# Optimization experiments

Measured on AMD Instinct MI355X. Metric: run time of the kernel, lower is better.

The kernel has to match this reference:

```python
import jax, jax.numpy as jnp
import numpy as np

B, S, T = 64, 24, 96
V, E, H, A = 32000, 256, 512, 512


def setup_inputs() -> dict:
    key = jax.random.key(0)
    ks = jax.random.split(key, 16)
    captions = jax.random.randint(ks[0], (B, S, T), 0, V)
    lengths = jax.random.randint(ks[1], (B, S), 1, T + 1)
    lengths = lengths.at[0].set(T)  # ensure per-sentence max length == T (matches dynamic seq_len_k)
    update_masks = jnp.arange(T)[None, None, :] < lengths[:, :, None]  # [B,S,T] bool prefix mask
    p = lambda k, shp: jax.random.normal(k, shp, dtype=jnp.float32) * 0.05
    return dict(
        captions=captions, update_masks=update_masks,
        embed_W=p(ks[2], (V, E)),
        w_Wih=p(ks[3], (4 * H, E)), w_Whh=p(ks[4], (4 * H, H)),
        w_bih=p(ks[5], (4 * H,)), w_bhh=p(ks[6], (4 * H,)),
        s_Wih=p(ks[7], (4 * H, H)), s_Whh=p(ks[8], (4 * H, H)),
        s_bih=p(ks[9], (4 * H,)), s_bhh=p(ks[10], (4 * H,)),
        wa_Wk=p(ks[11], (A, H)), wa_Wv=p(ks[12], (1, A)),
        sa_Wk=p(ks[13], (A, H)), sa_Wv=p(ks[14], (1, A)),
    )


def _lstm_cell(x, h, c, Wih, Whh, bih, bhh):
    # torch.nn.LSTMCell gate order: i, f, g, o
    g = x @ Wih.T + bih + h @ Whh.T + bhh
    i, f, gg, o = jnp.split(g, 4, axis=-1)
    c2 = jax.nn.sigmoid(f) * c + jax.nn.sigmoid(i) * jnp.tanh(gg)
    h2 = jax.nn.sigmoid(o) * jnp.tanh(c2)
    return h2, c2


def _attn(k, Wk, Wv):
    # SelfAttention: softmax(affine(tanh(affine_k(k)))) pooled context
    z = (jnp.tanh(k @ Wk.T) @ Wv.T)[..., 0]          # [B,L]
    alpha = jax.nn.softmax(z, axis=1)
    ctx = jnp.einsum('blh,bl->bh', k, alpha)
    return ctx, alpha


def reference(captions, update_masks, embed_W, w_Wih, w_Whh, w_bih, w_bhh,
              s_Wih, s_Whh, s_bih, s_bhh, wa_Wk, wa_Wv, sa_Wk, sa_Wv):
    emb = embed_W[captions]                            # [B,S,T,E]
    bsz = captions.shape[0]
    zeros = jnp.zeros((bsz, H), jnp.float32)

    def sent_step(carry, ins):
        sh, sc, wh, wc = carry
        emb_k, m_k = ins                               # [B,T,E], [B,T]

        def word_step(c2, inp):
            wh_, wc_ = c2
            x, m = inp                                 # [B,E], [B] bool
            nh, nc = _lstm_cell(x, wh_, wc_, w_Wih, w_Whh, w_bih, w_bhh)
            m1 = m[:, None]
            # masked state update; inactive positions store 0 in word_hs
            return (jnp.where(m1, nh, wh_), jnp.where(m1, nc, wc_)), jnp.where(m1, nh, 0.0)

        (wh, wc), hs = jax.lax.scan(word_step, (wh, wc),
                                    (emb_k.transpose(1, 0, 2), m_k.T))
        word_hs = hs.transpose(1, 0, 2)                # [B,T,H]
        ctx, _ = _attn(word_hs, wa_Wk, wa_Wv)
        sh, sc = _lstm_cell(ctx, sh, sc, s_Wih, s_Whh, s_bih, s_bhh)
        return (sh, sc, wh, wc), sh

    _, sent_hs = jax.lax.scan(sent_step, (zeros, zeros, zeros, zeros),
                              (emb.transpose(1, 0, 2, 3), update_masks.transpose(1, 0, 2)))
    sent_hs = sent_hs.transpose(1, 0, 2)               # [B,S,H]
    context, alpha = _attn(sent_hs, sa_Wk, sa_Wv)
    return context, alpha
```

## Files before the change

### kernel.cpp

```cpp
#include <hip/hip_runtime.h>
#include <hip/hip_cooperative_groups.h>
#include <math.h>

namespace cg = cooperative_groups;

constexpr int kB = 64, kS = 24, kT = 96, kE = 256, kH = 512, kA = 512;
constexpr int NWG = 256, NTH = 512;
constexpr int NG = 8, GWG = 32, GB = 8;
constexpr int WHP = 516;
constexpr int HSP = 580;
constexpr int EMP = 264;
constexpr int EMB0 = 4640;
constexpr int ATP = 516;

constexpr int OFF_PUB = 0;
constexpr int OFF_SH  = OFF_PUB + 2 * NG * GWG * 128;
constexpr int OFF_HS  = OFF_SH + 2 * kB * kH;
constexpr int OFF_Z   = OFF_HS + kB * kT * kH;
constexpr int OFF_CTX = OFF_Z + kB * kT;
constexpr int OFF_SHS = OFF_CTX + kB * kH;
constexpr int OFF_Z2  = OFF_SHS + kB * kS * kH;
constexpr int OFF_FLG = (OFF_Z2 + kB * kS + 31) & ~31;

typedef float f4v __attribute__((ext_vector_type(4)));

__device__ __forceinline__ float sigmoidf(float x) { return 1.0f / (1.0f + expf(-x)); }
__device__ __forceinline__ float dot4(float4 a, float4 b) {
  return a.x * b.x + a.y * b.y + a.z * b.z + a.w * b.w;
}
__device__ __forceinline__ float2 aload2(const float* p) {
  unsigned long long u = __hip_atomic_load((const unsigned long long*)p,
                                           __ATOMIC_RELAXED, __HIP_MEMORY_SCOPE_AGENT);
  union { unsigned long long u; float2 f; } cv; cv.u = u;
  return cv.f;
}
__device__ __forceinline__ float aload1(const float* p) {
  return __hip_atomic_load(p, __ATOMIC_RELAXED, __HIP_MEMORY_SCOPE_AGENT);
}
__device__ __forceinline__ void astore(float* p, float v) {
  __hip_atomic_store(p, v, __ATOMIC_RELAXED, __HIP_MEMORY_SCOPE_AGENT);
}
__device__ __forceinline__ unsigned aloadu(const unsigned* p) {
  return __hip_atomic_load(p, __ATOMIC_RELAXED, __HIP_MEMORY_SCOPE_AGENT);
}
__device__ __forceinline__ void astoreu(unsigned* p, unsigned v) {
  __hip_atomic_store(p, v, __ATOMIC_RELAXED, __HIP_MEMORY_SCOPE_AGENT);
}
__device__ __forceinline__ unsigned l2_loadu(const unsigned* p) {
  unsigned r;
  asm volatile("global_load_dword %0, %1, off sc0\n\ts_waitcnt vmcnt(0)"
               : "=v"(r) : "v"(p) : "memory");
  return r;
}
__device__ __forceinline__ float l2_load1(const float* p) {
  float r;
  asm volatile("global_load_dword %0, %1, off sc0\n\ts_waitcnt vmcnt(0)"
               : "=v"(r) : "v"(p) : "memory");
  return r;
}
__device__ __forceinline__ float2 l2_load2(const float* p) {
  float2 r;
  asm volatile("global_load_dwordx2 %0, %1, off sc0\n\ts_waitcnt vmcnt(0)"
               : "=v"(r) : "v"(p) : "memory");
  return r;
}
__device__ __forceinline__ void l2_load8(const float* p, f4v& a, f4v& b) {
  asm volatile("global_load_dwordx4 %0, %2, off sc0\n\t"
               "global_load_dwordx4 %1, %2, off offset:16 sc0\n\t"
               "s_waitcnt vmcnt(0)"
               : "=&v"(a), "=&v"(b) : "v"(p) : "memory");
}
__device__ __forceinline__ void l2_atomic_inc(unsigned* p) {
  unsigned one = 1u;
  asm volatile("global_atomic_add %0, %1, off" :: "v"(p), "v"(one) : "memory");
}

__global__ __launch_bounds__(NTH) void ha_kernel(
    const int* __restrict__ captions, const int* __restrict__ masks,
    const float* __restrict__ embed_W,
    const float* __restrict__ w_Wih, const float* __restrict__ w_Whh,
    const float* __restrict__ w_bih, const float* __restrict__ w_bhh,
    const float* __restrict__ s_Wih, const float* __restrict__ s_Whh,
    const float* __restrict__ s_bih, const float* __restrict__ s_bhh,
    const float* __restrict__ wa_Wk, const float* __restrict__ wa_Wv,
    const float* __restrict__ sa_Wk, const float* __restrict__ sa_Wv,
    float* __restrict__ out, float* __restrict__ ws) {
  cg::grid_group grid = cg::this_grid();
  const int g = blockIdx.x, tid = threadIdx.x;
  const int jj = tid >> 6, c = tid & 63;

  float* pub = ws + OFF_PUB;
  float* sh_buf = ws + OFF_SH;
  float* hs_buf = ws + OFF_HS;
  float* z_buf = ws + OFF_Z;
  float* ctx_ws = ws + OFF_CTX;
  float* sent_hs = ws + OFF_SHS;
  float* z2_buf = ws + OFF_Z2;
  unsigned* flags = (unsigned*)(ws + OFF_FLG);
  unsigned* cntp = flags + 8192;
  unsigned* tflagA = flags + 8448;
  unsigned* tdataA = flags + 8704;
  unsigned* verdA = flags + 8960;

  __shared__ __align__(16) float whh_s[64 * WHP];
  __shared__ __align__(16) float uni[6752];
  __shared__ float bias_s[64];
  __shared__ float c_s[16][8], hown_s[16][8], sc_s[16][8];
  __shared__ unsigned mbits[24];
  __shared__ float soft_s[96], red_s[96];
  __shared__ int ibuf[4];

  {
    int idx = g * NTH + tid;
    if (idx < 2 * kB * kH) sh_buf[idx] = 0.f;
  }
  if (g == 0)
    for (int idx = tid; idx < 9216; idx += NTH) flags[idx] = 0u;
  grid.sync();

  if (tid == 0) {
    unsigned xcc;
    asm volatile("s_getreg_b32 %0, hwreg(20, 0, 32)" : "=s"(xcc));
    xcc &= 7u;
    unsigned slot = atomicAdd(&cntp[xcc * 32], 1u);
    ibuf[0] = (int)xcc; ibuf[1] = (int)slot;
  }
  grid.sync();
  __syncthreads();
  const int myxcc = ibuf[0], myslot = ibuf[1];
  unsigned cnts[8]; int px[9]; px[0] = 0;
  for (int x = 0; x < 8; ++x) { cnts[x] = aloadu(&cntp[x * 32]); px[x + 1] = px[x] + (int)cnts[x]; }
  const int rank = px[myxcc] + myslot;
  const int grp = rank >> 5, r = rank & 31;
  const int B0 = GB * grp;
  bool pure = false;
  for (int x = 0; x < 8; ++x)
    if (px[x] <= grp * 32 && grp * 32 + 32 <= px[x + 1]) pure = true;
  const bool cand = pure && (cnts[myxcc] <= 40u);
  unsigned* myflag = &flags[(grp * GWG + r) * 32];

  auto g_row = [&](int cc) { return (cc >> 4) * kH + 16 * r + (cc & 15); };

  unsigned n = 0;
  {
    unsigned* tf = &tflagA[grp * 32];
    unsigned* td = &tdataA[grp * 32];
    int ok = 0;
    if (cand && r == 0 && tid == 0) {
      *td = 0xC0FFEEu;
      asm volatile("s_waitcnt vmcnt(0)" ::: "memory");
      l2_atomic_inc(tf);
    }
    if (cand && tid == 0) {
      for (int it = 0; it < 4096; ++it) {
        if (l2_loadu(tf) >= 1u) { ok = (l2_loadu(td) == 0xC0FFEEu); break; }
        __builtin_amdgcn_s_sleep(2);
      }
    }
    if (tid == 0) {
      astoreu(&verdA[grp * 32 + r], ok ? 1u : 0u);
      asm volatile("s_waitcnt vmcnt(0)" ::: "memory");
      atomicAdd(myflag, 1u);
    }
    n = 1;
    if (tid < GWG) {
      while (aloadu(&flags[(grp * GWG + tid) * 32]) < 1u) __builtin_amdgcn_s_sleep(2);
    }
    __syncthreads();
    if (tid < GWG) red_s[tid] = (float)aloadu(&verdA[grp * 32 + tid]);
    __syncthreads();
    if (tid == 0) {
      int all = 1;
      for (int i = 0; i < GWG; ++i) all &= (red_s[i] != 0.f);
      ibuf[2] = all;
    }
    __syncthreads();
  }
  const bool l2m = (ibuf[2] != 0);

  auto mstore1 = [&](float* p, float v) { if (l2m) *p = v; else astore(p, v); };
  auto mload1 = [&](const float* p) { return l2m ? l2_load1(p) : aload1(p); };
  auto mload2 = [&](const float* p) { return l2m ? l2_load2(p) : aload2(p); };
  auto mload8 = [&](const float* p, f4v& a, f4v& b) {
    if (l2m) l2_load8(p, a, b);
    else {
      float2 t0 = aload2(p), t1 = aload2(p + 2), t2 = aload2(p + 4), t3 = aload2(p + 6);
      a = f4v{t0.x, t0.y, t1.x, t1.y}; b = f4v{t2.x, t2.y, t3.x, t3.y};
    }
  };
  auto arrive = [&]() {
    __syncthreads();
    if (tid == 0) { if (l2m) l2_atomic_inc(myflag); else atomicAdd(myflag, 1u); }
  };
  auto wait = [&](unsigned nn) {
    if (tid < GWG) {
      const unsigned* fp = &flags[(grp * GWG + tid) * 32];
      if (l2m) { while (l2_loadu(fp) < nn) __builtin_amdgcn_s_sleep(1); }
      else     { while (aloadu(fp) < nn)   __builtin_amdgcn_s_sleep(1); }
    }
    __syncthreads();
  };

  for (int idx = tid; idx < 64 * kH; idx += NTH) {
    const int c2 = idx >> 9, kk = idx & 511;
    whh_s[c2 * WHP + 4 * (((kk >> 2) + 4 * (c2 & 1)) & 127) + (kk & 3)] =
        w_Whh[(size_t)g_row(c2) * kH + kk];
  }
  if (tid < 64) bias_s[tid] = w_bih[g_row(tid)] + w_bhh[g_row(tid)];
  if (tid < 128) {
    c_s[tid >> 3][tid & 7] = 0.f; hown_s[tid >> 3][tid & 7] = 0.f; sc_s[tid >> 3][tid & 7] = 0.f;
  }
  for (int idx = tid; idx < 6752; idx += NTH) uni[idx] = 0.f;
  __syncthreads();

  auto stage_hst_pub = [&](const float* slab) {
    const int lin = tid * 8, rsm = lin >> 7, rem = lin & 127;
    const int b2 = rem >> 4, kk = (rsm << 4) | (rem & 15);
    f4v a, b4; mload8(slab + lin, a, b4);
    const int ho = kk + 4 * (kk >> 5);
    *(f4v*)&uni[b2 * HSP + ho] = a;
    *(f4v*)&uni[b2 * HSP + ho + 4] = b4;
  };
  auto stage_hst_lin = [&](const float* src) {
    const int lin = tid * 8, b2 = lin >> 9, kk = lin & 511;
    f4v a, b4; mload8(src + lin, a, b4);
    const int ho = kk + 4 * (kk >> 5);
    *(f4v*)&uni[b2 * HSP + ho] = a;
    *(f4v*)&uni[b2 * HSP + ho + 4] = b4;
  };
  auto stage_emb = [&](int s2, int t2) {
    const int b2 = tid >> 6, ch = tid & 63;
    const int cap = captions[((B0 + b2) * kS + s2) * kT + t2];
    const float4 v = *(const float4*)&embed_W[(size_t)cap * kE + 4 * ch];
    *(float4*)&uni[EMB0 + b2 * EMP + 4 * ch] = v;
  };
  float xp[8];
  auto calc_xp = [&]() {
    const float* wr = w_Wih + (size_t)g_row(c) * kE + 32 * jj;
    const float* eb = &uni[EMB0];
#pragma unroll
    for (int b2 = 0; b2 < 8; ++b2) xp[b2] = 0.f;
#pragma unroll
    for (int v = 0; v < 8; ++v) {
      const float4 w = *(const float4*)&wr[4 * v];
#pragma unroll
      for (int b2 = 0; b2 < 8; ++b2)
        xp[b2] += dot4(w, *(const float4*)&eb[b2 * EMP + 32 * jj + 4 * v]);
    }
  };

  stage_emb(0, 0);
  __syncthreads();
  calc_xp();

  int gstep = 0;
  for (int s = 0; s < kS; ++s) {
    if (tid < 24) {
      const int b2 = tid / 3, w2 = tid % 3;
      unsigned bits = 0u;
      const int base = ((B0 + b2) * kS + s) * kT + 32 * w2;
      for (int j = 0; j < 32; ++j) bits |= (masks[base + j] ? 1u : 0u) << j;
      mbits[b2 * 3 + w2] = bits;
    }
    if (s > 0) stage_hst_pub(pub + ((size_t)((gstep & 1) * NG + grp)) * 4096);
    __syncthreads();

    for (int t = 0; t < kT; ++t, ++gstep) {
      float* pubw = pub + ((size_t)(((gstep + 1) & 1) * NG + grp)) * 4096;

      float acc[8];
#pragma unroll
      for (int b2 = 0; b2 < 8; ++b2) acc[b2] = xp[b2];
      {
        const int swc = 4 * (c & 1);
        const float* wrow = &whh_s[c * WHP];
#pragma unroll 4
        for (int u = 0; u < 16; ++u) {
          const int q = 16 * jj + u;
          const float4 w = *(const float4*)&wrow[4 * ((q + swc) & 127)];
          const int hoff = 4 * q + 4 * (q >> 3);
#pragma unroll
          for (int b2 = 0; b2 < 8; ++b2)
            acc[b2] += dot4(w, *(const float4*)&uni[b2 * HSP + hoff]);
        }
      }
      __syncthreads();
#pragma unroll
      for (int b2 = 0; b2 < 8; ++b2) uni[jj * HSP + c * 9 + b2] = acc[b2];
      __syncthreads();
      float hsv = 0.f;
      if (tid < 128) {
        const int hcl = tid >> 3, b2 = tid & 7;
        float gg4[4];
#pragma unroll
        for (int g2 = 0; g2 < 4; ++g2) {
          const int c2 = g2 * 16 + hcl;
          float sum = bias_s[c2];
#pragma unroll
          for (int j = 0; j < 8; ++j) sum += uni[j * HSP + c2 * 9 + b2];
          gg4[g2] = sum;
        }
        const float cold = c_s[hcl][b2];
        const float c2v = sigmoidf(gg4[1]) * cold + sigmoidf(gg4[0]) * tanhf(gg4[2]);
        const float h2 = sigmoidf(gg4[3]) * tanhf(c2v);
        const int m = (mbits[b2 * 3 + (t >> 5)] >> (t & 31)) & 1;
        const float cn = m ? c2v : cold;
        const float hn = m ? h2 : hown_s[hcl][b2];
        c_s[hcl][b2] = cn; hown_s[hcl][b2] = hn;
        mstore1(&pubw[r * 128 + b2 * 16 + hcl], hn);
        hsv = m ? h2 : 0.f;
      }
      ++n;
      arrive();
      if (tid < 128) {
        const int hcl = tid >> 3, b2 = tid & 7;
        mstore1(&hs_buf[((size_t)(B0 + b2) * kT + t) * kH + 16 * r + hcl], hsv);
      }
      int ns = s, nt = t + 1; bool have = true;
      if (nt == kT) { nt = 0; ns = s + 1; if (ns == kS) have = false; }
      if (have) stage_emb(ns, nt);
      __syncthreads();
      if (have) calc_xp();
      wait(n);
      stage_hst_pub(pubw);
      __syncthreads();
    }

    ++n; arrive(); wait(n);

    {
      const int ab = r >> 2, t0 = (r & 3) * 24;
      const int bg = B0 + ab;
      for (int half = 0; half < 2; ++half) {
        const int tb = t0 + half * 12;
        for (int idx = tid; idx < 12 * 256; idx += NTH) {
          const int pp = idx >> 8, hh2 = (idx & 255) * 2;
          float2 v = mload2(&hs_buf[((size_t)bg * kT + tb + pp) * kH + hh2]);
          *(float2*)&uni[pp * ATP + hh2] = v;
        }
        __syncthreads();
        float dacc[12];
#pragma unroll
        for (int p = 0; p < 12; ++p) dacc[p] = 0.f;
        const float4* __restrict__ wk = (const float4*)(wa_Wk + (size_t)tid * kH);
        for (int k = 0; k < kH / 4; ++k) {
          const float4 w = wk[k];
#pragma unroll
          for (int p = 0; p < 12; ++p)
            dacc[p] += dot4(w, *(const float4*)&uni[p * ATP + 4 * k]);
        }
        const float wv = wa_Wv[tid];
        const int ln = tid & 63, wid = tid >> 6;
#pragma unroll
        for (int p = 0; p < 12; ++p) {
          float v = wv * tanhf(dacc[p]);
          v += __shfl_down(v, 32); v += __shfl_down(v, 16); v += __shfl_down(v, 8);
          v += __shfl_down(v, 4);  v += __shfl_down(v, 2);  v += __shfl_down(v, 1);
          if (ln == 0) red_s[wid * 12 + p] = v;
        }
        __syncthreads();
        if (tid < 12) {
          float sum = 0.f;
#pragma unroll
          for (int w = 0; w < 8; ++w) sum += red_s[w * 12 + tid];
          mstore1(&z_buf[bg * kT + tb + tid], sum);
        }
        __syncthreads();
      }
    }
    ++n; arrive(); wait(n);

    if (r < GB) {
      const int b2 = B0 + r;
      if (tid < kT) soft_s[tid] = mload1(&z_buf[b2 * kT + tid]);
      __syncthreads();
      float mx = -1e30f;
      for (int i = 0; i < kT; ++i) mx = fmaxf(mx, soft_s[i]);
      float den = 0.f;
      for (int i = 0; i < kT; ++i) den += expf(soft_s[i] - mx);
      __syncthreads();
      if (tid < kT) soft_s[tid] = expf(soft_s[tid] - mx) / den;
      __syncthreads();
      {
        const int h0 = tid;
        float a0 = 0.f, a1 = 0.f, a2 = 0.f, a3 = 0.f;
        for (int tt = 0; tt < kT; tt += 4) {
          a0 += soft_s[tt + 0] * mload1(&hs_buf[((size_t)b2 * kT + tt + 0) * kH + h0]);
          a1 += soft_s[tt + 1] * mload1(&hs_buf[((size_t)b2 * kT + tt + 1) * kH + h0]);
          a2 += soft_s[tt + 2] * mload1(&hs_buf[((size_t)b2 * kT + tt + 2) * kH + h0]);
          a3 += soft_s[tt + 3] * mload1(&hs_buf[((size_t)b2 * kT + tt + 3) * kH + h0]);
        }
        mstore1(&ctx_ws[b2 * kH + h0], (a0 + a1) + (a2 + a3));
      }
    }
    ++n; arrive(); wait(n);

    {
      float acc[8];
#pragma unroll
      for (int b2 = 0; b2 < 8; ++b2) acc[b2] = 0.f;
      stage_hst_lin(ctx_ws + B0 * kH);
      __syncthreads();
      {
        const float* wA = s_Wih + (size_t)g_row(c) * kH + 64 * jj;
#pragma unroll 8
        for (int u = 0; u < 16; ++u) {
          const float4 w = *(const float4*)&wA[4 * u];
          const int q = 16 * jj + u;
          const int hoff = 4 * q + 4 * (q >> 3);
#pragma unroll
          for (int b2 = 0; b2 < 8; ++b2)
            acc[b2] += dot4(w, *(const float4*)&uni[b2 * HSP + hoff]);
        }
      }
      __syncthreads();
      stage_hst_lin(sh_buf + (s & 1) * kB * kH + B0 * kH);
      __syncthreads();
      {
        const float* wB = s_Whh + (size_t)g_row(c) * kH + 64 * jj;
#pragma unroll 8
        for (int u = 0; u < 16; ++u) {
          const float4 w = *(const float4*)&wB[4 * u];
          const int q = 16 * jj + u;
          const int hoff = 4 * q + 4 * (q >> 3);
#pragma unroll
          for (int b2 = 0; b2 < 8; ++b2)
            acc[b2] += dot4(w, *(const float4*)&uni[b2 * HSP + hoff]);
        }
      }
      __syncthreads();
#pragma unroll
      for (int b2 = 0; b2 < 8; ++b2) uni[jj * HSP + c * 9 + b2] = acc[b2];
      __syncthreads();
      if (tid < 128) {
        const int hcl = tid >> 3, b2 = tid & 7;
        float gg4[4];
#pragma unroll
        for (int g2 = 0; g2 < 4; ++g2) {
          const int c2 = g2 * 16 + hcl;
          const int row = g_row(c2);
          float sum = s_bih[row] + s_bhh[row];
#pragma unroll
          for (int j = 0; j < 8; ++j) sum += uni[j * HSP + c2 * 9 + b2];
          gg4[g2] = sum;
        }
        const float c2v = sigmoidf(gg4[1]) * sc_s[hcl][b2] + sigmoidf(gg4[0]) * tanhf(gg4[2]);
        const float h2 = sigmoidf(gg4[3]) * tanhf(c2v);
        sc_s[hcl][b2] = c2v;
        const int col = 16 * r + hcl;
        mstore1(&sh_buf[((s + 1) & 1) * kB * kH + (B0 + b2) * kH + col], h2);
        mstore1(&sent_hs[((size_t)(B0 + b2) * kS + s) * kH + col], h2);
      }
    }
    ++n; arrive(); wait(n);
  }

  {
    const int pair0 = r * 6;
    for (int idx = tid; idx < 6 * 256; idx += NTH) {
      const int pp = idx >> 8, hh2 = (idx & 255) * 2;
      const int pr = pair0 + pp;
      float2 v = mload2(&sent_hs[((size_t)(B0 + pr / kS) * kS + pr % kS) * kH + hh2]);
      *(float2*)&uni[pp * ATP + hh2] = v;
    }
    __syncthreads();
    float dacc[6];
#pragma unroll
    for (int p = 0; p < 6; ++p) dacc[p] = 0.f;
    const float4* __restrict__ wk = (const float4*)(sa_Wk + (size_t)tid * kH);
    for (int k = 0; k < kH / 4; ++k) {
      const float4 w = wk[k];
#pragma unroll
      for (int p = 0; p < 6; ++p)
        dacc[p] += dot4(w, *(const float4*)&uni[p * ATP + 4 * k]);
    }
    const float wv = sa_Wv[tid];
    const int ln = tid & 63, wid = tid >> 6;
#pragma unroll
    for (int p = 0; p < 6; ++p) {
      float v = wv * tanhf(dacc[p]);
      v += __shfl_down(v, 32); v += __shfl_down(v, 16); v += __shfl_down(v, 8);
      v += __shfl_down(v, 4);  v += __shfl_down(v, 2);  v += __shfl_down(v, 1);
      if (ln == 0) red_s[wid * 6 + p] = v;
    }
    __syncthreads();
    if (tid < 6) {
      float sum = 0.f;
#pragma unroll
      for (int w = 0; w < 8; ++w) sum += red_s[w * 6 + tid];
      mstore1(&z2_buf[B0 * kS + pair0 + tid], sum);
    }
  }
  ++n; arrive(); wait(n);

  if (r < GB) {
    const int b2 = B0 + r;
    if (tid < kS) soft_s[tid] = mload1(&z2_buf[b2 * kS + tid]);
    __syncthreads();
    float mx = -1e30f;
    for (int i = 0; i < kS; ++i) mx = fmaxf(mx, soft_s[i]);
    float den = 0.f;
    for (int i = 0; i < kS; ++i) den += expf(soft_s[i] - mx);
    __syncthreads();
    if (tid < kS) {
      const float al = expf(soft_s[tid] - mx) / den;
      soft_s[tid] = al;
      out[kB * kH + b2 * kS + tid] = al;
    }
    __syncthreads();
    {
      const int h0 = tid;
      float acc2 = 0.f;
      for (int s2 = 0; s2 < kS; ++s2)
        acc2 += soft_s[s2] * mload1(&sent_hs[((size_t)b2 * kS + s2) * kH + h0]);
      out[b2 * kH + h0] = acc2;
    }
  }
}

extern "C" void kernel_launch(void* const* d_in, const int* in_sizes, int n_in,
                              void* d_out, int out_size, void* d_ws, size_t ws_size,
                              hipStream_t stream) {
  (void)in_sizes; (void)n_in; (void)out_size; (void)ws_size;
  const int* captions = (const int*)d_in[0];
  const int* masks = (const int*)d_in[1];
  const float* embed_W = (const float*)d_in[2];
  const float* w_Wih = (const float*)d_in[3];
  const float* w_Whh = (const float*)d_in[4];
  const float* w_bih = (const float*)d_in[5];
  const float* w_bhh = (const float*)d_in[6];
  const float* s_Wih = (const float*)d_in[7];
  const float* s_Whh = (const float*)d_in[8];
  const float* s_bih = (const float*)d_in[9];
  const float* s_bhh = (const float*)d_in[10];
  const float* wa_Wk = (const float*)d_in[11];
  const float* wa_Wv = (const float*)d_in[12];
  const float* sa_Wk = (const float*)d_in[13];
  const float* sa_Wv = (const float*)d_in[14];
  float* out = (float*)d_out;
  float* ws = (float*)d_ws;

  void* args[] = {&captions, &masks, &embed_W, &w_Wih, &w_Whh, &w_bih, &w_bhh,
                  &s_Wih, &s_Whh, &s_bih, &s_bhh, &wa_Wk, &wa_Wv, &sa_Wk, &sa_Wv,
                  &out, &ws};
  hipLaunchCooperativeKernel((void*)ha_kernel, dim3(NWG), dim3(NTH), args, 0, stream);
}
```

Measured before the change: 25.08 ms.

## Register-tile two gate rows per thread in word LSTM recurrence and batch L2 loads

Each thread in the per-timestep Whh matvec now computes two gate rows (c2 and c2+32) over half the K range, so every LDS load of the hidden state feeds two dot products. The two K halves are combined with a cross-half shuffle before the existing reduction. The input-projection weight slice is held in registers across timesteps instead of being reloaded from global memory each step. In the attention context loop, four L2 loads are issued back-to-back before one wait instead of four separate waits. The cost is higher register pressure from the doubled accumulators and the cached weights.

```diff
diff --git a/kernel.cpp b/kernel.cpp
--- a/kernel.cpp
+++ b/kernel.cpp
@@ -69,6 +69,17 @@
                "global_load_dwordx4 %1, %2, off offset:16 sc0\n\t"
                "s_waitcnt vmcnt(0)"
                : "=&v"(a), "=&v"(b) : "v"(p) : "memory");
+}
+__device__ __forceinline__ void l2_load4s(const float* p0, const float* p1,
+                                          const float* p2, const float* p3,
+                                          float& r0, float& r1, float& r2, float& r3) {
+  asm volatile("global_load_dword %0, %4, off sc0\n\t"
+               "global_load_dword %1, %5, off sc0\n\t"
+               "global_load_dword %2, %6, off sc0\n\t"
+               "global_load_dword %3, %7, off sc0\n\t"
+               "s_waitcnt vmcnt(0)"
+               : "=&v"(r0), "=&v"(r1), "=&v"(r2), "=&v"(r3)
+               : "v"(p0), "v"(p1), "v"(p2), "v"(p3) : "memory");
 }
 __device__ __forceinline__ void l2_atomic_inc(unsigned* p) {
   unsigned one = 1u;
@@ -87,7 +98,11 @@
     float* __restrict__ out, float* __restrict__ ws) {
   cg::grid_group grid = cg::this_grid();
   const int g = blockIdx.x, tid = threadIdx.x;
-  const int jj = tid >> 6, c = tid & 63;
+  const int jj = tid >> 6;
+  const int c = tid & 63;
+  const int half = (tid >> 5) & 1;
+  const int c2 = tid & 31;
+  const int ks = jj * 2 + half;
 
   float* pub = ws + OFF_PUB;
   float* sh_buf = ws + OFF_SH;
@@ -188,6 +203,11 @@
       a = f4v{t0.x, t0.y, t1.x, t1.y}; b = f4v{t2.x, t2.y, t3.x, t3.y};
     }
   };
+  auto mload4s = [&](const float* p0, const float* p1, const float* p2, const float* p3,
+                     float& r0, float& r1, float& r2, float& r3) {
+    if (l2m) l2_load4s(p0, p1, p2, p3, r0, r1, r2, r3);
+    else { r0 = aload1(p0); r1 = aload1(p1); r2 = aload1(p2); r3 = aload1(p3); }
+  };
   auto arrive = [&]() {
     __syncthreads();
     if (tid == 0) { if (l2m) l2_atomic_inc(myflag); else atomicAdd(myflag, 1u); }
@@ -202,15 +222,25 @@
   };
 
   for (int idx = tid; idx < 64 * kH; idx += NTH) {
-    const int c2 = idx >> 9, kk = idx & 511;
-    whh_s[c2 * WHP + 4 * (((kk >> 2) + 4 * (c2 & 1)) & 127) + (kk & 3)] =
-        w_Whh[(size_t)g_row(c2) * kH + kk];
+    const int cr = idx >> 9, kk = idx & 511;
+    whh_s[cr * WHP + 4 * (((kk >> 2) + 4 * (cr & 1)) & 127) + (kk & 3)] =
+        w_Whh[(size_t)g_row(cr) * kH + kk];
   }
   if (tid < 64) bias_s[tid] = w_bih[g_row(tid)] + w_bhh[g_row(tid)];
   if (tid < 128) {
     c_s[tid >> 3][tid & 7] = 0.f; hown_s[tid >> 3][tid & 7] = 0.f; sc_s[tid >> 3][tid & 7] = 0.f;
   }
   for (int idx = tid; idx < 6752; idx += NTH) uni[idx] = 0.f;
+  float4 wir0[4], wir1[4];
+  {
+    const float* wrA = w_Wih + (size_t)g_row(c2) * kE + 16 * ks;
+    const float* wrB = w_Wih + (size_t)g_row(c2 + 32) * kE + 16 * ks;
+#pragma unroll
+    for (int v = 0; v < 4; ++v) {
+      wir0[v] = *(const float4*)&wrA[4 * v];
+      wir1[v] = *(const float4*)&wrB[4 * v];
+    }
+  }
   __syncthreads();
 
   auto stage_hst_pub = [&](const float* slab) {
@@ -234,18 +264,19 @@
     const float4 v = *(const float4*)&embed_W[(size_t)cap * kE + 4 * ch];
     *(float4*)&uni[EMB0 + b2 * EMP + 4 * ch] = v;
   };
-  float xp[8];
+  float xp0[8], xp1[8];
   auto calc_xp = [&]() {
-    const float* wr = w_Wih + (size_t)g_row(c) * kE + 32 * jj;
-    const float* eb = &uni[EMB0];
-#pragma unroll
-    for (int b2 = 0; b2 < 8; ++b2) xp[b2] = 0.f;
-#pragma unroll
-    for (int v = 0; v < 8; ++v) {
-      const float4 w = *(const float4*)&wr[4 * v];
-#pragma unroll
-      for (int b2 = 0; b2 < 8; ++b2)
-        xp[b2] += dot4(w, *(const float4*)&eb[b2 * EMP + 32 * jj + 4 * v]);
+    const float* eb = &uni[EMB0 + 16 * ks];
+#pragma unroll
+    for (int b2 = 0; b2 < 8; ++b2) { xp0[b2] = 0.f; xp1[b2] = 0.f; }
+#pragma unroll
+    for (int v = 0; v < 4; ++v) {
+#pragma unroll
+      for (int b2 = 0; b2 < 8; ++b2) {
+        const float4 ev = *(const float4*)&eb[b2 * EMP + 4 * v];
+        xp0[b2] += dot4(wir0[v], ev);
+        xp1[b2] += dot4(wir1[v], ev);
+      }
     }
   };
 
@@ -268,25 +299,34 @@
     for (int t = 0; t < kT; ++t, ++gstep) {
       float* pubw = pub + ((size_t)(((gstep + 1) & 1) * NG + grp)) * 4096;
 
-      float acc[8];
-#pragma unroll
-      for (int b2 = 0; b2 < 8; ++b2) acc[b2] = xp[b2];
+      float acc0[8], acc1[8];
+#pragma unroll
+      for (int b2 = 0; b2 < 8; ++b2) { acc0[b2] = xp0[b2]; acc1[b2] = xp1[b2]; }
       {
-        const int swc = 4 * (c & 1);
-        const float* wrow = &whh_s[c * WHP];
-#pragma unroll 4
-        for (int u = 0; u < 16; ++u) {
-          const int q = 16 * jj + u;
-          const float4 w = *(const float4*)&wrow[4 * ((q + swc) & 127)];
+        const int swc = 4 * (c2 & 1);
+        const float* w0 = &whh_s[c2 * WHP];
+        const float* w1 = &whh_s[(c2 + 32) * WHP];
+#pragma unroll
+        for (int u = 0; u < 8; ++u) {
+          const int q = 8 * ks + u;
+          const float4 wv0 = *(const float4*)&w0[4 * ((q + swc) & 127)];
+          const float4 wv1 = *(const float4*)&w1[4 * ((q + swc) & 127)];
           const int hoff = 4 * q + 4 * (q >> 3);
 #pragma unroll
-          for (int b2 = 0; b2 < 8; ++b2)
-            acc[b2] += dot4(w, *(const float4*)&uni[b2 * HSP + hoff]);
-        }
-      }
-      __syncthreads();
-#pragma unroll
-      for (int b2 = 0; b2 < 8; ++b2) uni[jj * HSP + c * 9 + b2] = acc[b2];
+          for (int b2 = 0; b2 < 8; ++b2) {
+            const float4 hv = *(const float4*)&uni[b2 * HSP + hoff];
+            acc0[b2] += dot4(wv0, hv);
+            acc1[b2] += dot4(wv1, hv);
+          }
+        }
+      }
+      __syncthreads();
+#pragma unroll
+      for (int b2 = 0; b2 < 8; ++b2) {
+        const float t0 = acc0[b2] + __shfl_xor(acc0[b2], 32);
+        const float t1 = acc1[b2] + __shfl_xor(acc1[b2], 32);
+        uni[jj * HSP + (c2 + 32 * half) * 9 + b2] = half ? t1 : t0;
+      }
       __syncthreads();
       float hsv = 0.f;
       if (tid < 128) {
@@ -294,10 +334,10 @@
         float gg4[4];
 #pragma unroll
         for (int g2 = 0; g2 < 4; ++g2) {
-          const int c2 = g2 * 16 + hcl;
-          float sum = bias_s[c2];
-#pragma unroll
-          for (int j = 0; j < 8; ++j) sum += uni[j * HSP + c2 * 9 + b2];
+          const int cc = g2 * 16 + hcl;
+          float sum = bias_s[cc];
+#pragma unroll
+          for (int j = 0; j < 8; ++j) sum += uni[j * HSP + cc * 9 + b2];
           gg4[g2] = sum;
         }
         const float cold = c_s[hcl][b2];
@@ -331,8 +371,8 @@
     {
       const int ab = r >> 2, t0 = (r & 3) * 24;
       const int bg = B0 + ab;
-      for (int half = 0; half < 2; ++half) {
-        const int tb = t0 + half * 12;
+      for (int halfp = 0; halfp < 2; ++halfp) {
+        const int tb = t0 + halfp * 12;
         for (int idx = tid; idx < 12 * 256; idx += NTH) {
           const int pp = idx >> 8, hh2 = (idx & 255) * 2;
           float2 v = mload2(&hs_buf[((size_t)bg * kT + tb + pp) * kH + hh2]);
@@ -385,10 +425,13 @@
         const int h0 = tid;
         float a0 = 0.f, a1 = 0.f, a2 = 0.f, a3 = 0.f;
         for (int tt = 0; tt < kT; tt += 4) {
-          a0 += soft_s[tt + 0] * mload1(&hs_buf[((size_t)b2 * kT + tt + 0) * kH + h0]);
-          a1 += soft_s[tt + 1] * mload1(&hs_buf[((size_t)b2 * kT + tt + 1) * kH + h0]);
-          a2 += soft_s[tt + 2] * mload1(&hs_buf[((size_t)b2 * kT + tt + 2) * kH + h0]);
-          a3 += soft_s[tt + 3] * mload1(&hs_buf[((size_t)b2 * kT + tt + 3) * kH + h0]);
+          const float* p = &hs_buf[((size_t)b2 * kT + tt) * kH + h0];
+          float v0, v1, v2, v3;
+          mload4s(p, p + kH, p + 2 * kH, p + 3 * kH, v0, v1, v2, v3);
+          a0 += soft_s[tt + 0] * v0;
+          a1 += soft_s[tt + 1] * v1;
+          a2 += soft_s[tt + 2] * v2;
+          a3 += soft_s[tt + 3] * v3;
         }
         mstore1(&ctx_ws[b2 * kH + h0], (a0 + a1) + (a2 + a3));
       }
@@ -437,11 +480,11 @@
         float gg4[4];
 #pragma unroll
         for (int g2 = 0; g2 < 4; ++g2) {
-          const int c2 = g2 * 16 + hcl;
-          const int row = g_row(c2);
+          const int cc = g2 * 16 + hcl;
+          const int row = g_row(cc);
           float sum = s_bih[row] + s_bhh[row];
 #pragma unroll
-          for (int j = 0; j < 8; ++j) sum += uni[j * HSP + c2 * 9 + b2];
+          for (int j = 0; j < 8; ++j) sum += uni[j * HSP + cc * 9 + b2];
           gg4[g2] = sum;
         }
         const float c2v = sigmoidf(gg4[1]) * sc_s[hcl][b2] + sigmoidf(gg4[0]) * tanhf(gg4[2]);
```

Result: slower. 30.03 ms (+19.7%).
